# Kernel tuning notes

Measured on AMD Instinct MI355X. Metric: run time of the kernel, lower is better.

The kernel has to match this reference:

```python
import jax, jax.numpy as jnp
import numpy as np
from jax import lax

WIN = 11
SIGMA = 1.5
C1 = 0.01 ** 2  # L = 1 (inputs in [0,1], matches pytorch_msssim dynamic-range inference)
C2 = 0.03 ** 2
WEIGHTS = np.array([0.0448, 0.2856, 0.3001, 0.2363, 0.1333], dtype=np.float32)


def _gauss_window(channels, dtype):
    x = np.arange(WIN, dtype=np.float64) - WIN // 2
    g = np.exp(-(x ** 2) / (2.0 * SIGMA ** 2))
    g = g / g.sum()
    w2d = np.outer(g, g).astype(np.float32)          # (11,11)
    w = np.broadcast_to(w2d, (channels, 1, WIN, WIN))  # depthwise OIHW
    return jnp.asarray(w, dtype=dtype)


def _dwconv(x, w):
    # depthwise valid conv, NCHW
    return lax.conv_general_dilated(
        x, w, window_strides=(1, 1), padding='VALID',
        dimension_numbers=('NCHW', 'OIHW', 'NCHW'),
        feature_group_count=x.shape[1])


def _ssim(img1, img2, w):
    mu1 = _dwconv(img1, w)
    mu2 = _dwconv(img2, w)
    mu1_sq, mu2_sq, mu1_mu2 = mu1 * mu1, mu2 * mu2, mu1 * mu2
    sigma1_sq = _dwconv(img1 * img1, w) - mu1_sq
    sigma2_sq = _dwconv(img2 * img2, w) - mu2_sq
    sigma12 = _dwconv(img1 * img2, w) - mu1_mu2
    v1 = 2.0 * sigma12 + C2
    v2 = sigma1_sq + sigma2_sq + C2
    cs = jnp.mean(v1 / v2)
    ssim_map = ((2.0 * mu1_mu2 + C1) * v1) / ((mu1_sq + mu2_sq + C1) * v2)
    return jnp.mean(ssim_map), cs


def _avgpool2(x):
    B, C, H, W = x.shape
    return x.reshape(B, C, H // 2, 2, W // 2, 2).mean(axis=(3, 5))


def _msssim(img1, img2):
    w = _gauss_window(img1.shape[1], img1.dtype)
    weights = jnp.asarray(WEIGHTS, dtype=img1.dtype)
    mssim, mcs = [], []
    for _ in range(len(WEIGHTS)):  # 5 fixed pyramid levels
        s, c = _ssim(img1, img2, w)
        mssim.append(s)
        mcs.append(c)
        img1, img2 = _avgpool2(img1), _avgpool2(img2)
    mssim = jnp.stack(mssim)
    mcs = jnp.stack(mcs)
    pow1 = mcs ** weights
    pow2 = mssim ** weights
    # literal translation of pytorch_msssim: torch.prod(pow1[:-1] * pow2[-1])
    return jnp.prod(pow1[:-1] * pow2[-1])


def setup_inputs() -> dict:
    key = jax.random.key(0)
    k1, k2 = jax.random.split(key)
    shape = (16, 3, 512, 512)
    reconst = jax.random.uniform(k1, shape, dtype=jnp.float32)
    original = jax.random.uniform(k2, shape, dtype=jnp.float32)
    return {"reconst": reconst, "original": original}


def reference(reconst, original):
    msssim = _msssim(original, reconst)
    mse = jnp.mean((original - reconst) ** 2)
    loss = mse - msssim + 1.0
    return (loss, msssim)
```

## Files before the change

kernel.cpp:

```cpp
#include <hip/hip_runtime.h>
#include <math.h>


#define NPLANES 48

struct GaussW { float g[11]; };

typedef float v2f __attribute__((ext_vector_type(2)));

#define PYR2_OFF  4177920
#define P_L0      8355840
#define P_L1      8358912
#define P_L2      8360448
#define P_L3      8361216
#define P_L4      8361408
#define P_MSE     8361480

#define C1F 1.0e-4f
#define C2F 9.0e-4f

template <int LOGW, int BH, int DO_MSE, int DO_POOL>
__global__ __launch_bounds__(256, 4) void ssim_band(
    const float* __restrict__ x1, const float* __restrict__ x2, GaussW gw,
    float* __restrict__ partials, float* __restrict__ msep,
    float* __restrict__ d1, float* __restrict__ d2)
{
  constexpr int W = 1 << LOGW;
  constexpr int Ho = W - 10;
  constexpr int LOGWB = (LOGW > 8) ? 8 : LOGW;
  constexpr int WB = 1 << LOGWB;
  constexpr int P = 256 >> LOGWB;
  constexpr int STRIDE = WB + 12;
  constexpr int W2 = W >> 1;

  __shared__ v2f vbuf[3][P][STRIDE];
  __shared__ float red[3][4];

  const int tid = threadIdx.x;
  const int p = tid >> LOGWB;
  const int col = tid & (WB - 1);
  const int bx = blockIdx.x, by = blockIdx.y, bz = blockIdx.z;
  const int gcol = bx * WB + col;
  const int plane = bz * P + p;
  const size_t pb = (size_t)plane * W * W;
  const float* q1 = x1 + pb + gcol;
  const float* q2 = x2 + pb + gcol;
  const int gr0 = BH * by;
  const int ROWS = ((W - gr0) < (BH + 10)) ? (W - gr0) : (BH + 10);
  const bool xtra = (bx * WB + WB + col) < W;

  float acc0[11], acc1[11], acc2[11], acc3[11], acc4[11];
#pragma unroll
  for (int j = 0; j < 11; ++j) {
    acc0[j] = 0.f; acc1[j] = 0.f; acc2[j] = 0.f; acc3[j] = 0.f; acc4[j] = 0.f;
  }

  float mse_acc = 0.f, ssim_acc = 0.f, cs_acc = 0.f;

  {
    size_t ro = (size_t)gr0 * W;
    float a = q1[ro], b = q2[ro];
    float ae = 0.f, be = 0.f;
    if (col < 12 && xtra) { ae = q1[ro + WB]; be = q2[ro + WB]; }
    if (DO_MSE) { float d = a - b; mse_acc = d * d; }
    vbuf[0][p][col] = (v2f){a, b};
    if (col < 12) vbuf[0][p][WB + col] = (v2f){ae, be};
  }
  __syncthreads();

  int cur = 0;
  for (int rr = 0; rr < ROWS; ++rr) {
    int nxt = cur + 1; if (nxt == 3) nxt = 0;
    int prv = cur - 1; if (prv < 0) prv = 2;
    const bool have = (rr + 1) < ROWS;

    float a = 0.f, b = 0.f, ae = 0.f, be = 0.f;
    if (have) {
      size_t ro = (size_t)(gr0 + rr + 1) * W;
      a = q1[ro]; b = q2[ro];
      if (col < 12 && xtra) { ae = q1[ro + WB]; be = q2[ro + WB]; }
    }

    const v2f* r = &vbuf[cur][p][col];
    float s1 = 0.f, s2 = 0.f, s11 = 0.f, s22 = 0.f, s12 = 0.f;
#pragma unroll
    for (int k = 0; k < 11; ++k) {
      v2f ab = r[k];
      float av = ab.x, bv = ab.y, w = gw.g[k];
      float wa = w * av, wb = w * bv;
      s1 += wa; s2 += wb;
      s11 = fmaf(wa, av, s11);
      s22 = fmaf(wb, bv, s22);
      s12 = fmaf(wa, bv, s12);
    }

#pragma unroll
    for (int j = 10; j >= 1; --j) {
      acc0[j] = fmaf(gw.g[j], s1, acc0[j - 1]);
      acc1[j] = fmaf(gw.g[j], s2, acc1[j - 1]);
      acc2[j] = fmaf(gw.g[j], s11, acc2[j - 1]);
      acc3[j] = fmaf(gw.g[j], s22, acc3[j - 1]);
      acc4[j] = fmaf(gw.g[j], s12, acc4[j - 1]);
    }
    acc0[0] = gw.g[0] * s1;
    acc1[0] = gw.g[0] * s2;
    acc2[0] = gw.g[0] * s11;
    acc3[0] = gw.g[0] * s22;
    acc4[0] = gw.g[0] * s12;

    if (rr >= 10 && gcol < Ho) {
      float m1 = acc0[10], m2 = acc1[10];
      float m1sq = m1 * m1, m2sq = m2 * m2, m12 = m1 * m2;
      float v1 = 2.f * (acc4[10] - m12) + C2F;
      float v2 = (acc2[10] - m1sq) + (acc3[10] - m2sq) + C2F;
      float csv = v1 * __builtin_amdgcn_rcpf(v2);
      cs_acc += csv;
      ssim_acc += csv * (2.f * m12 + C1F) *
                  __builtin_amdgcn_rcpf(m1sq + m2sq + C1F);
    }

    if (DO_POOL && (rr & 1) && rr < BH && col < (WB / 2)) {
      v2f x0 = vbuf[prv][p][2 * col], x1v = vbuf[prv][p][2 * col + 1];
      v2f y0 = vbuf[cur][p][2 * col], y1v = vbuf[cur][p][2 * col + 1];
      int orow = (gr0 >> 1) + (rr >> 1);
      size_t ob = (size_t)plane * W2 * W2 + (size_t)orow * W2 + bx * (WB / 2) + col;
      d1[ob] = 0.25f * ((x0.x + x1v.x) + (y0.x + y1v.x));
      d2[ob] = 0.25f * ((x0.y + x1v.y) + (y0.y + y1v.y));
    }

    if (have) {
      if (DO_MSE && (rr + 1) < BH) { float d = a - b; mse_acc = fmaf(d, d, mse_acc); }
      vbuf[nxt][p][col] = (v2f){a, b};
      if (col < 12) vbuf[nxt][p][WB + col] = (v2f){ae, be};
      __syncthreads();
    }
    cur = nxt;
  }

#pragma unroll
  for (int off = 32; off; off >>= 1) {
    ssim_acc += __shfl_down(ssim_acc, off);
    cs_acc += __shfl_down(cs_acc, off);
    if (DO_MSE) mse_acc += __shfl_down(mse_acc, off);
  }
  int wave = tid >> 6, lane = tid & 63;
  if (lane == 0) {
    red[0][wave] = ssim_acc;
    red[1][wave] = cs_acc;
    if (DO_MSE) red[2][wave] = mse_acc;
  }
  __syncthreads();
  if (tid == 0) {
    float s = 0.f, cc = 0.f, m = 0.f;
#pragma unroll
    for (int i = 0; i < 4; ++i) {
      s += red[0][i];
      cc += red[1][i];
      if (DO_MSE) m += red[2][i];
    }
    int bi = (bz * gridDim.y + by) * gridDim.x + bx;
    partials[2 * bi] = s;
    partials[2 * bi + 1] = cc;
    if (DO_MSE) msep[bi] = m;
  }
}

__global__ __launch_bounds__(256) void final_kernel(
    const float* __restrict__ ws, float* __restrict__ out)
{
  __shared__ double sred[2][4];
  __shared__ double fin[11];
  const int tid = threadIdx.x;
  const int offs[5] = {P_L0, P_L1, P_L2, P_L3, P_L4};
  const int cnts[5] = {1536, 768, 384, 96, 36};

  for (int l = 0; l < 5; ++l) {
    double s0 = 0.0, s1 = 0.0;
    for (int i = tid; i < cnts[l]; i += 256) {
      s0 += (double)ws[offs[l] + 2 * i];
      s1 += (double)ws[offs[l] + 2 * i + 1];
    }
#pragma unroll
    for (int off = 32; off; off >>= 1) {
      s0 += __shfl_down(s0, off);
      s1 += __shfl_down(s1, off);
    }
    if ((tid & 63) == 0) { sred[0][tid >> 6] = s0; sred[1][tid >> 6] = s1; }
    __syncthreads();
    if (tid == 0) {
      double aa = 0.0, bb = 0.0;
      for (int i = 0; i < 4; ++i) { aa += sred[0][i]; bb += sred[1][i]; }
      fin[l] = aa;
      fin[5 + l] = bb;
    }
    __syncthreads();
  }

  {
    double s0 = 0.0;
    for (int i = tid; i < 1536; i += 256) s0 += (double)ws[P_MSE + i];
#pragma unroll
    for (int off = 32; off; off >>= 1) s0 += __shfl_down(s0, off);
    if ((tid & 63) == 0) sred[0][tid >> 6] = s0;
    __syncthreads();
    if (tid == 0) {
      double aa = 0.0;
      for (int i = 0; i < 4; ++i) aa += sred[0][i];
      fin[10] = aa;
    }
    __syncthreads();
  }

  if (tid == 0) {
    const double wts[5] = {0.0448, 0.2856, 0.3001, 0.2363, 0.1333};
    const double dims[5] = {502.0, 246.0, 118.0, 54.0, 22.0};
    double mssim[5], mcs[5];
    for (int l = 0; l < 5; ++l) {
      double n = 48.0 * dims[l] * dims[l];
      mssim[l] = fin[l] / n;
      mcs[l] = fin[5 + l] / n;
    }
    double p2last = pow(mssim[4], wts[4]);
    double prod = 1.0;
    for (int i = 0; i < 4; ++i) prod *= pow(mcs[i], wts[i]) * p2last;
    double msssim = prod;
    double mse = fin[10] / 12582912.0;
    out[0] = (float)(mse - msssim + 1.0);
    out[1] = (float)msssim;
  }
}

extern "C" void kernel_launch(void* const* d_in, const int* in_sizes, int n_in,
                              void* d_out, int out_size, void* d_ws, size_t ws_size,
                              hipStream_t stream)
{
  const float* rec = (const float*)d_in[0];
  const float* orig = (const float*)d_in[1];
  float* ws = (float*)d_ws;
  float* out = (float*)d_out;

  GaussW gw;
  {
    double g[11], s = 0.0;
    for (int i = 0; i < 11; ++i) {
      double x = (double)i - 5.0;
      g[i] = exp(-(x * x) / 4.5);
      s += g[i];
    }
    for (int i = 0; i < 11; ++i) gw.g[i] = (float)(g[i] / s);
  }

  float* A1 = ws + 0;
  float* A2 = ws + 3145728;
  float* A3 = ws + 3932160;
  float* A4 = ws + 4128768;
  float* B1 = ws + PYR2_OFF;
  float* B2 = ws + PYR2_OFF + 3145728;
  float* B3 = ws + PYR2_OFF + 3932160;
  float* B4 = ws + PYR2_OFF + 4128768;

  ssim_band<9, 32, 1, 1><<<dim3(2, 16, 48), 256, 0, stream>>>(
      orig, rec, gw, ws + P_L0, ws + P_MSE, A1, B1);
  ssim_band<8, 16, 0, 1><<<dim3(1, 16, 48), 256, 0, stream>>>(
      A1, B1, gw, ws + P_L1, nullptr, A2, B2);
  ssim_band<7, 8, 0, 1><<<dim3(1, 16, 24), 256, 0, stream>>>(
      A2, B2, gw, ws + P_L2, nullptr, A3, B3);
  ssim_band<6, 8, 0, 1><<<dim3(1, 8, 12), 256, 0, stream>>>(
      A3, B3, gw, ws + P_L3, nullptr, A4, B4);
  ssim_band<5, 4, 0, 0><<<dim3(1, 6, 6), 256, 0, stream>>>(
      A4, B4, gw, ws + P_L4, nullptr, nullptr, nullptr);

  final_kernel<<<dim3(1), dim3(256), 0, stream>>>(ws, out);
}
```

Baseline: 143.4 us.

## Process two rows per barrier and merge squared-sum sliding accumulators

Measured after the change: 152.0 us. 1.06x slower.

```diff
diff --git a/kernel.cpp b/kernel.cpp
--- a/kernel.cpp
+++ b/kernel.cpp
@@ -33,7 +33,7 @@
   constexpr int STRIDE = WB + 12;
   constexpr int W2 = W >> 1;
 
-  __shared__ v2f vbuf[3][P][STRIDE];
+  __shared__ v2f vbuf[4][P][STRIDE];
   __shared__ float red[3][4];
 
   const int tid = threadIdx.x;
@@ -49,93 +49,110 @@
   const int ROWS = ((W - gr0) < (BH + 10)) ? (W - gr0) : (BH + 10);
   const bool xtra = (bx * WB + WB + col) < W;
 
-  float acc0[11], acc1[11], acc2[11], acc3[11], acc4[11];
-#pragma unroll
-  for (int j = 0; j < 11; ++j) {
-    acc0[j] = 0.f; acc1[j] = 0.f; acc2[j] = 0.f; acc3[j] = 0.f; acc4[j] = 0.f;
-  }
+  float f1[11], f2[11], f3[11], f4[11];
+#pragma unroll
+  for (int j = 0; j < 11; ++j) { f1[j] = 0.f; f2[j] = 0.f; f3[j] = 0.f; f4[j] = 0.f; }
 
   float mse_acc = 0.f, ssim_acc = 0.f, cs_acc = 0.f;
 
+#define LOADR(R, a, b, ae, be)                                          \
+  {                                                                     \
+    a = 0.f; b = 0.f; ae = 0.f; be = 0.f;                               \
+    {                                                                   \
+      size_t ro = (size_t)(gr0 + (R)) * W;                              \
+      a = q1[ro]; b = q2[ro];                                           \
+      if (col < 12 && xtra) { ae = q1[ro + WB]; be = q2[ro + WB]; }     \
+      if (DO_MSE && (R) < BH) {                                         \
+        float d_ = a - b;                                               \
+        mse_acc = fmaf(d_, d_, mse_acc);                                \
+      }                                                                 \
+    }                                                                   \
+  }
+
+#define STAGE(R, a, b, ae, be)                                          \
+  {                                                                     \
+    const int sl_ = (R) & 3;                                            \
+    vbuf[sl_][p][col] = (v2f){a, b};                                    \
+    if (col < 12) vbuf[sl_][p][WB + col] = (v2f){ae, be};               \
+  }
+
+#define PROW(R)                                                         \
+  {                                                                     \
+    const v2f* r_ = &vbuf[(R) & 3][p][col];                             \
+    float s1 = 0.f, s2 = 0.f, s3 = 0.f, s4 = 0.f;                       \
+    _Pragma("unroll") for (int k = 0; k < 11; ++k) {                    \
+      v2f ab = r_[k];                                                   \
+      float av = ab.x, bv = ab.y, w = gw.g[k];                          \
+      float wa = w * av, wb = w * bv;                                   \
+      s1 += wa; s2 += wb;                                               \
+      s3 = fmaf(wa, bv, s3);                                            \
+      s4 = fmaf(wa, av, s4);                                            \
+      s4 = fmaf(wb, bv, s4);                                            \
+    }                                                                   \
+    _Pragma("unroll") for (int j = 10; j >= 1; --j) {                   \
+      f1[j] = fmaf(gw.g[j], s1, f1[j - 1]);                             \
+      f2[j] = fmaf(gw.g[j], s2, f2[j - 1]);                             \
+      f3[j] = fmaf(gw.g[j], s3, f3[j - 1]);                             \
+      f4[j] = fmaf(gw.g[j], s4, f4[j - 1]);                             \
+    }                                                                   \
+    f1[0] = gw.g[0] * s1;                                               \
+    f2[0] = gw.g[0] * s2;                                               \
+    f3[0] = gw.g[0] * s3;                                               \
+    f4[0] = gw.g[0] * s4;                                               \
+    if ((R) >= 10 && gcol < Ho) {                                       \
+      float m1 = f1[10], m2 = f2[10], e12 = f3[10], esq = f4[10];       \
+      float m12 = m1 * m2;                                              \
+      float msq = fmaf(m1, m1, m2 * m2);                                \
+      float v1 = 2.f * (e12 - m12) + C2F;                               \
+      float vv2 = (esq - msq) + C2F;                                    \
+      float csv = v1 * __builtin_amdgcn_rcpf(vv2);                      \
+      cs_acc += csv;                                                    \
+      ssim_acc += csv * (2.f * m12 + C1F) *                             \
+                  __builtin_amdgcn_rcpf(msq + C1F);                     \
+    }                                                                   \
+  }
+
   {
-    size_t ro = (size_t)gr0 * W;
-    float a = q1[ro], b = q2[ro];
-    float ae = 0.f, be = 0.f;
-    if (col < 12 && xtra) { ae = q1[ro + WB]; be = q2[ro + WB]; }
-    if (DO_MSE) { float d = a - b; mse_acc = d * d; }
-    vbuf[0][p][col] = (v2f){a, b};
-    if (col < 12) vbuf[0][p][WB + col] = (v2f){ae, be};
+    float a0, b0, ae0, be0, a1, b1, ae1, be1;
+    LOADR(0, a0, b0, ae0, be0)
+    LOADR(1, a1, b1, ae1, be1)
+    STAGE(0, a0, b0, ae0, be0)
+    STAGE(1, a1, b1, ae1, be1)
   }
   __syncthreads();
 
-  int cur = 0;
-  for (int rr = 0; rr < ROWS; ++rr) {
-    int nxt = cur + 1; if (nxt == 3) nxt = 0;
-    int prv = cur - 1; if (prv < 0) prv = 2;
-    const bool have = (rr + 1) < ROWS;
-
-    float a = 0.f, b = 0.f, ae = 0.f, be = 0.f;
+  for (int i = 0; i < ROWS / 2; ++i) {
+    const int r0 = 2 * i, r1 = 2 * i + 1;
+    const bool have = (r0 + 2) < ROWS;
+
+    float na0 = 0.f, nb0 = 0.f, nae0 = 0.f, nbe0 = 0.f;
+    float na1 = 0.f, nb1 = 0.f, nae1 = 0.f, nbe1 = 0.f;
     if (have) {
-      size_t ro = (size_t)(gr0 + rr + 1) * W;
-      a = q1[ro]; b = q2[ro];
-      if (col < 12 && xtra) { ae = q1[ro + WB]; be = q2[ro + WB]; }
-    }
-
-    const v2f* r = &vbuf[cur][p][col];
-    float s1 = 0.f, s2 = 0.f, s11 = 0.f, s22 = 0.f, s12 = 0.f;
-#pragma unroll
-    for (int k = 0; k < 11; ++k) {
-      v2f ab = r[k];
-      float av = ab.x, bv = ab.y, w = gw.g[k];
-      float wa = w * av, wb = w * bv;
-      s1 += wa; s2 += wb;
-      s11 = fmaf(wa, av, s11);
-      s22 = fmaf(wb, bv, s22);
-      s12 = fmaf(wa, bv, s12);
-    }
-
-#pragma unroll
-    for (int j = 10; j >= 1; --j) {
-      acc0[j] = fmaf(gw.g[j], s1, acc0[j - 1]);
-      acc1[j] = fmaf(gw.g[j], s2, acc1[j - 1]);
-      acc2[j] = fmaf(gw.g[j], s11, acc2[j - 1]);
-      acc3[j] = fmaf(gw.g[j], s22, acc3[j - 1]);
-      acc4[j] = fmaf(gw.g[j], s12, acc4[j - 1]);
-    }
-    acc0[0] = gw.g[0] * s1;
-    acc1[0] = gw.g[0] * s2;
-    acc2[0] = gw.g[0] * s11;
-    acc3[0] = gw.g[0] * s22;
-    acc4[0] = gw.g[0] * s12;
-
-    if (rr >= 10 && gcol < Ho) {
-      float m1 = acc0[10], m2 = acc1[10];
-      float m1sq = m1 * m1, m2sq = m2 * m2, m12 = m1 * m2;
-      float v1 = 2.f * (acc4[10] - m12) + C2F;
-      float v2 = (acc2[10] - m1sq) + (acc3[10] - m2sq) + C2F;
-      float csv = v1 * __builtin_amdgcn_rcpf(v2);
-      cs_acc += csv;
-      ssim_acc += csv * (2.f * m12 + C1F) *
-                  __builtin_amdgcn_rcpf(m1sq + m2sq + C1F);
-    }
-
-    if (DO_POOL && (rr & 1) && rr < BH && col < (WB / 2)) {
-      v2f x0 = vbuf[prv][p][2 * col], x1v = vbuf[prv][p][2 * col + 1];
-      v2f y0 = vbuf[cur][p][2 * col], y1v = vbuf[cur][p][2 * col + 1];
-      int orow = (gr0 >> 1) + (rr >> 1);
+      LOADR(r0 + 2, na0, nb0, nae0, nbe0)
+      LOADR(r1 + 2, na1, nb1, nae1, nbe1)
+    }
+
+    PROW(r0)
+    PROW(r1)
+
+    if (DO_POOL && r0 < BH && col < (WB / 2)) {
+      v2f x0 = vbuf[r0 & 3][p][2 * col], x1v = vbuf[r0 & 3][p][2 * col + 1];
+      v2f y0 = vbuf[r1 & 3][p][2 * col], y1v = vbuf[r1 & 3][p][2 * col + 1];
+      int orow = (gr0 >> 1) + i;
       size_t ob = (size_t)plane * W2 * W2 + (size_t)orow * W2 + bx * (WB / 2) + col;
       d1[ob] = 0.25f * ((x0.x + x1v.x) + (y0.x + y1v.x));
       d2[ob] = 0.25f * ((x0.y + x1v.y) + (y0.y + y1v.y));
     }
 
     if (have) {
-      if (DO_MSE && (rr + 1) < BH) { float d = a - b; mse_acc = fmaf(d, d, mse_acc); }
-      vbuf[nxt][p][col] = (v2f){a, b};
-      if (col < 12) vbuf[nxt][p][WB + col] = (v2f){ae, be};
+      STAGE(r0 + 2, na0, nb0, nae0, nbe0)
+      STAGE(r1 + 2, na1, nb1, nae1, nbe1)
       __syncthreads();
     }
-    cur = nxt;
-  }
+  }
+#undef LOADR
+#undef STAGE
+#undef PROW
 
 #pragma unroll
   for (int off = 32; off; off >>= 1) {
```

## Give level-0 SSIM its own full-row kernel with two columns per thread

Applied to the files above, without the earlier changes.

New measurement: 545.3 us. 3.8x slower.

```diff
diff --git a/kernel.cpp b/kernel.cpp
--- a/kernel.cpp
+++ b/kernel.cpp
@@ -10,19 +10,190 @@
 
 #define PYR2_OFF  4177920
 #define P_L0      8355840
-#define P_L1      8358912
-#define P_L2      8360448
-#define P_L3      8361216
-#define P_L4      8361408
-#define P_MSE     8361480
+#define P_L1      8357376
+#define P_L2      8358912
+#define P_L3      8359680
+#define P_L4      8359872
+#define P_MSE     8359944
 
 #define C1F 1.0e-4f
 #define C2F 9.0e-4f
 
-template <int LOGW, int BH, int DO_MSE, int DO_POOL>
+__global__ __launch_bounds__(256, 4) void ssim_l0(
+    const float* __restrict__ x1, const float* __restrict__ x2, GaussW gw,
+    float* __restrict__ partials, float* __restrict__ msep,
+    float* __restrict__ d1, float* __restrict__ d2)
+{
+  constexpr int W = 512, Ho = 502, BH = 32, W2 = 256;
+  constexpr int STRIDE = 524;
+
+  __shared__ v2f vbuf[3][STRIDE];
+  __shared__ float red[3][4];
+
+  const int tid = threadIdx.x;
+  const int by = blockIdx.x;
+  const int plane = blockIdx.y;
+  const int gr0 = BH * by;
+  const int ROWS = ((W - gr0) < (BH + 10)) ? (W - gr0) : (BH + 10);
+  const int c0 = tid, c1 = tid + 256;
+  const size_t pb = (size_t)plane * W * W;
+
+  if (tid < 12) {
+    vbuf[0][512 + tid] = (v2f){0.f, 0.f};
+    vbuf[1][512 + tid] = (v2f){0.f, 0.f};
+    vbuf[2][512 + tid] = (v2f){0.f, 0.f};
+  }
+
+  float f1[11], f2[11], f3[11], f4[11];
+  float h1[11], h2[11], h3[11], h4[11];
+#pragma unroll
+  for (int j = 0; j < 11; ++j) {
+    f1[j] = 0.f; f2[j] = 0.f; f3[j] = 0.f; f4[j] = 0.f;
+    h1[j] = 0.f; h2[j] = 0.f; h3[j] = 0.f; h4[j] = 0.f;
+  }
+
+  float mse_acc = 0.f, ssim_acc = 0.f, cs_acc = 0.f;
+
+  {
+    size_t ro = pb + (size_t)gr0 * W;
+    float a0 = x1[ro + c0], b0 = x2[ro + c0];
+    float a1 = x1[ro + c1], b1 = x2[ro + c1];
+    float d0 = a0 - b0, d1_ = a1 - b1;
+    mse_acc = fmaf(d0, d0, d1_ * d1_);
+    vbuf[0][c0] = (v2f){a0, b0};
+    vbuf[0][c1] = (v2f){a1, b1};
+  }
+  __syncthreads();
+
+  int cur = 0;
+  for (int rr = 0; rr < ROWS; ++rr) {
+    int nxt = cur + 1; if (nxt == 3) nxt = 0;
+    int prv = cur - 1; if (prv < 0) prv = 2;
+    const bool have = (rr + 1) < ROWS;
+
+    float a0 = 0.f, b0 = 0.f, a1 = 0.f, b1 = 0.f;
+    if (have) {
+      size_t ro = pb + (size_t)(gr0 + rr + 1) * W;
+      a0 = x1[ro + c0]; b0 = x2[ro + c0];
+      a1 = x1[ro + c1]; b1 = x2[ro + c1];
+    }
+
+    const v2f* r0 = &vbuf[cur][c0];
+    const v2f* r1 = &vbuf[cur][c1];
+    float s1 = 0.f, s2 = 0.f, s3 = 0.f, s4 = 0.f;
+    float t1 = 0.f, t2 = 0.f, t3 = 0.f, t4 = 0.f;
+#pragma unroll
+    for (int k = 0; k < 11; ++k) {
+      float w = gw.g[k];
+      {
+        v2f ab = r0[k];
+        float wa = w * ab.x, wb = w * ab.y;
+        s1 += wa; s2 += wb;
+        s3 = fmaf(wa, ab.y, s3);
+        s4 = fmaf(wa, ab.x, s4);
+        s4 = fmaf(wb, ab.y, s4);
+      }
+      {
+        v2f ab = r1[k];
+        float wa = w * ab.x, wb = w * ab.y;
+        t1 += wa; t2 += wb;
+        t3 = fmaf(wa, ab.y, t3);
+        t4 = fmaf(wa, ab.x, t4);
+        t4 = fmaf(wb, ab.y, t4);
+      }
+    }
+
+#pragma unroll
+    for (int j = 10; j >= 1; --j) {
+      f1[j] = fmaf(gw.g[j], s1, f1[j - 1]);
+      f2[j] = fmaf(gw.g[j], s2, f2[j - 1]);
+      f3[j] = fmaf(gw.g[j], s3, f3[j - 1]);
+      f4[j] = fmaf(gw.g[j], s4, f4[j - 1]);
+      h1[j] = fmaf(gw.g[j], t1, h1[j - 1]);
+      h2[j] = fmaf(gw.g[j], t2, h2[j - 1]);
+      h3[j] = fmaf(gw.g[j], t3, h3[j - 1]);
+      h4[j] = fmaf(gw.g[j], t4, h4[j - 1]);
+    }
+    f1[0] = gw.g[0] * s1; f2[0] = gw.g[0] * s2;
+    f3[0] = gw.g[0] * s3; f4[0] = gw.g[0] * s4;
+    h1[0] = gw.g[0] * t1; h2[0] = gw.g[0] * t2;
+    h3[0] = gw.g[0] * t3; h4[0] = gw.g[0] * t4;
+
+    if (rr >= 10) {
+      {
+        float m1 = f1[10], m2 = f2[10], e12 = f3[10], esq = f4[10];
+        float m12 = m1 * m2;
+        float msq = fmaf(m1, m1, m2 * m2);
+        float v1 = 2.f * (e12 - m12) + C2F;
+        float vv2 = (esq - msq) + C2F;
+        float csv = v1 * __builtin_amdgcn_rcpf(vv2);
+        cs_acc += csv;
+        ssim_acc += csv * (2.f * m12 + C1F) *
+                    __builtin_amdgcn_rcpf(msq + C1F);
+      }
+      if (tid < 246) {
+        float m1 = h1[10], m2 = h2[10], e12 = h3[10], esq = h4[10];
+        float m12 = m1 * m2;
+        float msq = fmaf(m1, m1, m2 * m2);
+        float v1 = 2.f * (e12 - m12) + C2F;
+        float vv2 = (esq - msq) + C2F;
+        float csv = v1 * __builtin_amdgcn_rcpf(vv2);
+        cs_acc += csv;
+        ssim_acc += csv * (2.f * m12 + C1F) *
+                    __builtin_amdgcn_rcpf(msq + C1F);
+      }
+    }
+
+    if ((rr & 1) && rr < BH) {
+      v2f x0 = vbuf[prv][2 * tid], x1v = vbuf[prv][2 * tid + 1];
+      v2f y0 = vbuf[cur][2 * tid], y1v = vbuf[cur][2 * tid + 1];
+      int orow = (gr0 >> 1) + (rr >> 1);
+      size_t ob = (size_t)plane * W2 * W2 + (size_t)orow * W2 + tid;
+      d1[ob] = 0.25f * ((x0.x + x1v.x) + (y0.x + y1v.x));
+      d2[ob] = 0.25f * ((x0.y + x1v.y) + (y0.y + y1v.y));
+    }
+
+    if (have) {
+      if (rr + 1 < BH) {
+        float d0 = a0 - b0, d1_ = a1 - b1;
+        mse_acc = fmaf(d0, d0, mse_acc);
+        mse_acc = fmaf(d1_, d1_, mse_acc);
+      }
+      vbuf[nxt][c0] = (v2f){a0, b0};
+      vbuf[nxt][c1] = (v2f){a1, b1};
+      __syncthreads();
+    }
+    cur = nxt;
+  }
+
+#pragma unroll
+  for (int off = 32; off; off >>= 1) {
+    ssim_acc += __shfl_down(ssim_acc, off);
+    cs_acc += __shfl_down(cs_acc, off);
+    mse_acc += __shfl_down(mse_acc, off);
+  }
+  int wave = tid >> 6, lane = tid & 63;
+  if (lane == 0) {
+    red[0][wave] = ssim_acc;
+    red[1][wave] = cs_acc;
+    red[2][wave] = mse_acc;
+  }
+  __syncthreads();
+  if (tid == 0) {
+    float s = 0.f, cc = 0.f, m = 0.f;
+#pragma unroll
+    for (int i = 0; i < 4; ++i) { s += red[0][i]; cc += red[1][i]; m += red[2][i]; }
+    int bi = blockIdx.y * 16 + blockIdx.x;
+    partials[2 * bi] = s;
+    partials[2 * bi + 1] = cc;
+    msep[bi] = m;
+  }
+}
+
+template <int LOGW, int BH, int DO_POOL>
 __global__ __launch_bounds__(256, 4) void ssim_band(
     const float* __restrict__ x1, const float* __restrict__ x2, GaussW gw,
-    float* __restrict__ partials, float* __restrict__ msep,
+    float* __restrict__ partials,
     float* __restrict__ d1, float* __restrict__ d2)
 {
   constexpr int W = 1 << LOGW;
@@ -34,7 +205,7 @@
   constexpr int W2 = W >> 1;
 
   __shared__ v2f vbuf[3][P][STRIDE];
-  __shared__ float red[3][4];
+  __shared__ float red[2][4];
 
   const int tid = threadIdx.x;
   const int p = tid >> LOGWB;
@@ -55,14 +226,13 @@
     acc0[j] = 0.f; acc1[j] = 0.f; acc2[j] = 0.f; acc3[j] = 0.f; acc4[j] = 0.f;
   }
 
-  float mse_acc = 0.f, ssim_acc = 0.f, cs_acc = 0.f;
+  float ssim_acc = 0.f, cs_acc = 0.f;
 
   {
     size_t ro = (size_t)gr0 * W;
     float a = q1[ro], b = q2[ro];
     float ae = 0.f, be = 0.f;
     if (col < 12 && xtra) { ae = q1[ro + WB]; be = q2[ro + WB]; }
-    if (DO_MSE) { float d = a - b; mse_acc = d * d; }
     vbuf[0][p][col] = (v2f){a, b};
     if (col < 12) vbuf[0][p][WB + col] = (v2f){ae, be};
   }
@@ -129,7 +299,6 @@
     }
 
     if (have) {
-      if (DO_MSE && (rr + 1) < BH) { float d = a - b; mse_acc = fmaf(d, d, mse_acc); }
       vbuf[nxt][p][col] = (v2f){a, b};
       if (col < 12) vbuf[nxt][p][WB + col] = (v2f){ae, be};
       __syncthreads();
@@ -141,27 +310,20 @@
   for (int off = 32; off; off >>= 1) {
     ssim_acc += __shfl_down(ssim_acc, off);
     cs_acc += __shfl_down(cs_acc, off);
-    if (DO_MSE) mse_acc += __shfl_down(mse_acc, off);
   }
   int wave = tid >> 6, lane = tid & 63;
   if (lane == 0) {
     red[0][wave] = ssim_acc;
     red[1][wave] = cs_acc;
-    if (DO_MSE) red[2][wave] = mse_acc;
   }
   __syncthreads();
   if (tid == 0) {
-    float s = 0.f, cc = 0.f, m = 0.f;
-#pragma unroll
-    for (int i = 0; i < 4; ++i) {
-      s += red[0][i];
-      cc += red[1][i];
-      if (DO_MSE) m += red[2][i];
-    }
+    float s = 0.f, cc = 0.f;
+#pragma unroll
+    for (int i = 0; i < 4; ++i) { s += red[0][i]; cc += red[1][i]; }
     int bi = (bz * gridDim.y + by) * gridDim.x + bx;
     partials[2 * bi] = s;
     partials[2 * bi + 1] = cc;
-    if (DO_MSE) msep[bi] = m;
   }
 }
 
@@ -172,7 +334,7 @@
   __shared__ double fin[11];
   const int tid = threadIdx.x;
   const int offs[5] = {P_L0, P_L1, P_L2, P_L3, P_L4};
-  const int cnts[5] = {1536, 768, 384, 96, 36};
+  const int cnts[5] = {768, 768, 384, 96, 36};
 
   for (int l = 0; l < 5; ++l) {
     double s0 = 0.0, s1 = 0.0;
@@ -198,7 +360,7 @@
 
   {
     double s0 = 0.0;
-    for (int i = tid; i < 1536; i += 256) s0 += (double)ws[P_MSE + i];
+    for (int i = tid; i < 768; i += 256) s0 += (double)ws[P_MSE + i];
 #pragma unroll
     for (int off = 32; off; off >>= 1) s0 += __shfl_down(s0, off);
     if ((tid & 63) == 0) sred[0][tid >> 6] = s0;
@@ -259,16 +421,17 @@
   float* B3 = ws + PYR2_OFF + 3932160;
   float* B4 = ws + PYR2_OFF + 4128768;
 
-  ssim_band<9, 32, 1, 1><<<dim3(2, 16, 48), 256, 0, stream>>>(
+  ssim_l0<<<dim3(16, 48), 256, 0, stream>>>(
       orig, rec, gw, ws + P_L0, ws + P_MSE, A1, B1);
-  ssim_band<8, 16, 0, 1><<<dim3(1, 16, 48), 256, 0, stream>>>(
-      A1, B1, gw, ws + P_L1, nullptr, A2, B2);
-  ssim_band<7, 8, 0, 1><<<dim3(1, 16, 24), 256, 0, stream>>>(
-      A2, B2, gw, ws + P_L2, nullptr, A3, B3);
-  ssim_band<6, 8, 0, 1><<<dim3(1, 8, 12), 256, 0, stream>>>(
-      A3, B3, gw, ws + P_L3, nullptr, A4, B4);
-  ssim_band<5, 4, 0, 0><<<dim3(1, 6, 6), 256, 0, stream>>>(
-      A4, B4, gw, ws + P_L4, nullptr, nullptr, nullptr);
+
+  ssim_band<8, 16, 1><<<dim3(1, 16, 48), 256, 0, stream>>>(
+      A1, B1, gw, ws + P_L1, A2, B2);
+  ssim_band<7, 8, 1><<<dim3(1, 16, 24), 256, 0, stream>>>(
+      A2, B2, gw, ws + P_L2, A3, B3);
+  ssim_band<6, 8, 1><<<dim3(1, 8, 12), 256, 0, stream>>>(
+      A3, B3, gw, ws + P_L3, A4, B4);
+  ssim_band<5, 4, 0><<<dim3(1, 6, 6), 256, 0, stream>>>(
+      A4, B4, gw, ws + P_L4, nullptr, nullptr);
 
   final_kernel<<<dim3(1), dim3(256), 0, stream>>>(ws, out);
 }
```
